# Performance work log

Measured on AMD Instinct MI355X. Metric: run time of the kernel, lower is better.

## Reference

```python
import jax, jax.numpy as jnp
import numpy as np

PATCH_SIZE = [3, 5, 7]
PATCH_SEQ = [5, 7]
SEQ_SIZE = 6
WIN = 210
D_MODEL = 256
B, M = 8, 55
EPS = 1e-5


def _loo(p):
    # leave-one-out index matrix, row i = all indices except i -> (p, p-1)
    return np.array([[k for k in range(p) if k != i] for i in range(p)], dtype=np.int32)


def _mlp(x, W1, b1, W2, b2):
    # torch MLP: fc2(relu(fc1(x))), Linear weights are (out, in)
    h = jax.nn.relu(x @ W1.T + b1)
    return h @ W2.T + b2


def _forward(x, sP, nP, ssP, nsP):
    Bn, L, Mn = x.shape
    # RevIN 'norm' with fresh affine (weight=1, bias=0): identity affine; stats detached
    mean = jax.lax.stop_gradient(jnp.mean(x, axis=1, keepdims=True))
    std = jax.lax.stop_gradient(jnp.sqrt(jnp.var(x, axis=1, keepdims=True) + EPS))
    xn = (x - mean) / std
    xt = jnp.transpose(xn, (0, 2, 1)).reshape(Bn * Mn, L)  # (BM, L)
    sm, pm, ssr, psr = [], [], [], []
    for j, p in enumerate(PATCH_SIZE):
        n = L // p
        x3 = xt.reshape(Bn * Mn, p, n)  # l = r*n + k
        # size branch: leave-one-out over the p axis, blocks ordered i*n + k
        feat = jnp.transpose(x3[:, _loo(p), :], (0, 1, 3, 2)).reshape(Bn * Mn, L, p - 1)
        y = _mlp(feat, *sP[j])[..., 0]  # (BM, L)
        sm.append(jnp.transpose(y.reshape(Bn, Mn, L), (0, 2, 1)))
        # num branch: leave-one-out over the n axis of row l%p, leaving out column l//p
        g = _mlp(x3[:, :, _loo(n)], *nP[j])[..., 0]  # (BM, p, n)
        # torch cats over l (axis 0) then reshapes (B, M, L): flat order is (l, b, m)
        prior = jnp.transpose(g, (2, 1, 0)).reshape(Bn, Mn, L)  # faithful scrambled reshape
        pm.append(jnp.transpose(prior, (0, 2, 1)))
    s = SEQ_SIZE
    for j, p in enumerate(PATCH_SEQ):
        n = L // (p * s)
        x4 = xt.reshape(Bn * Mn, p, n, s)  # l = (r*n + k)*s + t
        # size_seq branch: leave-one-out over p, feature = (p-1)*s per (i, k) position
        feat = jnp.transpose(x4[:, _loo(p)], (0, 1, 3, 2, 4)).reshape(Bn * Mn, p * n, (p - 1) * s)
        y = _mlp(feat, *ssP[j])  # (BM, p*n, s)
        ssr.append(jnp.transpose(y.reshape(Bn, Mn, L), (0, 2, 1)))
        # num_seq branch: leave-one-out over n, cat order i*p + r
        featn = jnp.transpose(x4[:, :, _loo(n), :], (0, 2, 1, 3, 4)).reshape(Bn * Mn, n * p, (n - 1) * s)
        g = _mlp(featn, *nsP[j])  # (BM, n*p, s)
        d0 = PATCH_SEQ[0]  # original code hardcodes patch_seq[0] here
        h = jnp.transpose(g.reshape(Bn, Mn, (n * p) // d0, d0, s), (0, 1, 3, 2, 4)).reshape(Bn, Mn, L)
        psr.append(jnp.transpose(h, (0, 2, 1)))
    # original returns 4 lists of (B, L, M); stack all 10 for a single output
    return jnp.stack(sm + pm + ssr + psr, axis=0)


def setup_inputs() -> dict:
    key = jax.random.key(0)
    keys = iter(jax.random.split(key, 128))
    d = {"x": jax.random.normal(next(keys), (B, WIN, M), dtype=jnp.float32)}

    def lin(name, out_d, in_d):
        d[name + "W"] = jax.random.normal(next(keys), (out_d, in_d), dtype=jnp.float32) / np.float32(np.sqrt(in_d))
        d[name + "b"] = jax.random.normal(next(keys), (out_d,), dtype=jnp.float32) * np.float32(0.01)

    for j, p in enumerate(PATCH_SIZE):
        lin(f"s1_{j}", D_MODEL, p - 1)
        lin(f"s2_{j}", 1, D_MODEL)
        lin(f"n1_{j}", D_MODEL, WIN // p - 1)
        lin(f"n2_{j}", 1, D_MODEL)
    for j, p in enumerate(PATCH_SEQ):
        lin(f"ss1_{j}", D_MODEL, (p - 1) * SEQ_SIZE)
        lin(f"ss2_{j}", SEQ_SIZE, D_MODEL)
        lin(f"ns1_{j}", D_MODEL, WIN // p - SEQ_SIZE)
        lin(f"ns2_{j}", SEQ_SIZE, D_MODEL)
    return d


def reference(x, s1_0W, s1_0b, s2_0W, s2_0b, n1_0W, n1_0b, n2_0W, n2_0b,
              s1_1W, s1_1b, s2_1W, s2_1b, n1_1W, n1_1b, n2_1W, n2_1b,
              s1_2W, s1_2b, s2_2W, s2_2b, n1_2W, n1_2b, n2_2W, n2_2b,
              ss1_0W, ss1_0b, ss2_0W, ss2_0b, ns1_0W, ns1_0b, ns2_0W, ns2_0b,
              ss1_1W, ss1_1b, ss2_1W, ss2_1b, ns1_1W, ns1_1b, ns2_1W, ns2_1b):
    sP = [(s1_0W, s1_0b, s2_0W, s2_0b), (s1_1W, s1_1b, s2_1W, s2_1b), (s1_2W, s1_2b, s2_2W, s2_2b)]
    nP = [(n1_0W, n1_0b, n2_0W, n2_0b), (n1_1W, n1_1b, n2_1W, n2_1b), (n1_2W, n1_2b, n2_2W, n2_2b)]
    ssP = [(ss1_0W, ss1_0b, ss2_0W, ss2_0b), (ss1_1W, ss1_1b, ss2_1W, ss2_1b)]
    nsP = [(ns1_0W, ns1_0b, ns2_0W, ns2_0b), (ns1_1W, ns1_1b, ns2_1W, ns2_1b)]
    return _forward(x, sP, nP, ssP, nsP)
```

## Files before the change

### kernel.cpp

```cpp
#include <hip/hip_runtime.h>

#define LL  210
#define MM  55
#define NBM 440
#define DM  256
#define MLT 11550
#define BLM 92400

#define XTG_OFF  0
#define W1T_OFF  92400
#define REC_OFF  158704

__device__ __forceinline__ void fma4(float4& a, const float4 w, const float s) {
    a.x += w.x * s; a.y += w.y * s; a.z += w.z * s; a.w += w.w * s;
}
__device__ __forceinline__ void fms4(float4& a, const float4 w, const float s) {
    a.x -= w.x * s; a.y -= w.y * s; a.z -= w.z * s; a.w -= w.w * s;
}

__device__ __forceinline__ float bfly8(const float y[8], const int lane) {
    float z[4];
#pragma unroll
    for (int i = 0; i < 4; ++i) {
        float snd = (lane & 1) ? y[2*i] : y[2*i+1];
        float rcv = __shfl_xor(snd, 1, 64);
        z[i] = ((lane & 1) ? y[2*i+1] : y[2*i]) + rcv;
    }
    float u[2];
#pragma unroll
    for (int i = 0; i < 2; ++i) {
        float snd = (lane & 2) ? z[2*i] : z[2*i+1];
        float rcv = __shfl_xor(snd, 2, 64);
        u[i] = ((lane & 2) ? z[2*i+1] : z[2*i]) + rcv;
    }
    {
        float snd = (lane & 4) ? u[0] : u[1];
        float rcv = __shfl_xor(snd, 4, 64);
        float w = ((lane & 4) ? u[1] : u[0]) + rcv;
        w += __shfl_xor(w, 8, 64);
        w += __shfl_xor(w, 16, 64);
        w += __shfl_xor(w, 32, 64);
        return w;
    }
}

__global__ __launch_bounds__(256) void kprep(
        const float* __restrict__ x,
        const float* __restrict__ nw0, const float* __restrict__ nw1, const float* __restrict__ nw2,
        const float* __restrict__ ssw0, const float* __restrict__ ssw1,
        const float* __restrict__ nsw0, const float* __restrict__ nsw1,
        const float* __restrict__ s1W0, const float* __restrict__ s1b0, const float* __restrict__ s2W0,
        const float* __restrict__ s1W1, const float* __restrict__ s1b1, const float* __restrict__ s2W1,
        const float* __restrict__ s1W2, const float* __restrict__ s1b2, const float* __restrict__ s2W2,
        float* __restrict__ xtg, float* __restrict__ w1t, float* __restrict__ recs) {
    const int t = threadIdx.x;
    const int blk = blockIdx.x;
    if (blk < 55) {
        const int mi = t & 7, li = t >> 3;
        const int bm = blk * 8 + mi;
        const int b = bm / MM, m = bm - b * MM;
        const float* xp = x + b * MLT + m;
        float vr[7], s1 = 0.f, s2 = 0.f;
#pragma unroll
        for (int it = 0; it < 7; ++it) {
            const int l = li + 32 * it;
            const float v = (l < LL) ? xp[l * MM] : 0.f;
            vr[it] = v; s1 += v; s2 += v * v;
        }
        s1 += __shfl_xor(s1, 8, 64);  s2 += __shfl_xor(s2, 8, 64);
        s1 += __shfl_xor(s1, 16, 64); s2 += __shfl_xor(s2, 16, 64);
        s1 += __shfl_xor(s1, 32, 64); s2 += __shfl_xor(s2, 32, 64);
        __shared__ float red[2][4][8];
        const int wid = t >> 6, lane = t & 63;
        if (lane < 8) { red[0][wid][lane] = s1; red[1][wid][lane] = s2; }
        __syncthreads();
        const float S1 = red[0][0][mi] + red[0][1][mi] + red[0][2][mi] + red[0][3][mi];
        const float S2 = red[1][0][mi] + red[1][1][mi] + red[1][2][mi] + red[1][3][mi];
        const float mean = S1 * (1.f / 210.f);
        const float inv = rsqrtf(S2 * (1.f / 210.f) - mean * mean + 1e-5f);
        float* xo = xtg + blk * 1680 + mi;
#pragma unroll
        for (int it = 0; it < 7; ++it) {
            const int l = li + 32 * it;
            if (l < LL) xo[l * 8] = (vr[it] - mean) * inv;
        }
    } else if (blk < 55 + 259) {
        const int e = (blk - 55) * 256 + t;
        const int cg = e >> 8, d = e & 255;
        const float* src; int ind, c;
        if (cg < 69)       { src = nw0;  ind = 69; c = cg; }
        else if (cg < 110) { src = nw1;  ind = 41; c = cg - 69; }
        else if (cg < 139) { src = nw2;  ind = 29; c = cg - 110; }
        else if (cg < 163) { src = ssw0; ind = 24; c = cg - 139; }
        else if (cg < 199) { src = ssw1; ind = 36; c = cg - 163; }
        else if (cg < 235) { src = nsw0; ind = 36; c = cg - 199; }
        else               { src = nsw1; ind = 24; c = cg - 235; }
        w1t[cg * DM + d] = src[d * ind + c];
    } else {
        const int e = (blk - 55 - 259) * 256 + t;
        float v;
        if (e < 1024) {
            int d = e >> 2, c = e & 3;
            v = (c < 2) ? s1W0[d * 2 + c] : (c == 2 ? s1b0[d] : s2W0[d]);
        } else if (e < 3072) {
            int rel = e - 1024, d = rel >> 3, c = rel & 7;
            v = (c < 4) ? s1W1[d * 4 + c] : (c == 4 ? s1b1[d] : (c == 5 ? s2W1[d] : 0.f));
        } else {
            int rel = e - 3072, d = rel >> 3, c = rel & 7;
            v = (c < 6) ? s1W2[d * 6 + c] : (c == 6 ? s1b2[d] : s2W2[d]);
        }
        recs[e] = v;
    }
}

template <int IND>
__device__ __forceinline__ void ksize_body2(const float* __restrict__ xtg,
        const float* __restrict__ rec, const float* __restrict__ b2,
        int bm0, int j, float* __restrict__ out) {
    constexpr int N = LL / (IND + 1);
    const int t = threadIdx.x;
    if (t >= LL) return;
    const float* xs = xtg + (bm0 >> 3) * 1680 + (bm0 & 7);
    const int i = t / N, k = t - i * N;
    float2 f[IND];
#pragma unroll
    for (int idx = 0; idx < IND; ++idx) {
        const int row = idx + (idx >= i);
        f[idx] = *(const float2*)&xs[(row * N + k) * 8];
    }
    const float b2v = b2[0];
    float y0a = 0.f, y0b = 0.f, y1a = 0.f, y1b = 0.f;
    const float4* r4 = (const float4*)rec;
    if constexpr (IND == 2) {
#pragma unroll 8
        for (int d = 0; d < DM; d += 2) {
            const float4 a = r4[d], b = r4[d + 1];
            y0a += fmaxf(a.x * f[0].x + a.y * f[1].x + a.z, 0.f) * a.w;
            y1a += fmaxf(a.x * f[0].y + a.y * f[1].y + a.z, 0.f) * a.w;
            y0b += fmaxf(b.x * f[0].x + b.y * f[1].x + b.z, 0.f) * b.w;
            y1b += fmaxf(b.x * f[0].y + b.y * f[1].y + b.z, 0.f) * b.w;
        }
    } else if constexpr (IND == 4) {
#pragma unroll 8
        for (int d = 0; d < DM; d += 2) {
            const float4 a = r4[2*d], b = r4[2*d+1];
            const float4 c = r4[2*d+2], e = r4[2*d+3];
            y0a += fmaxf(a.x*f[0].x + a.y*f[1].x + a.z*f[2].x + a.w*f[3].x + b.x, 0.f) * b.y;
            y1a += fmaxf(a.x*f[0].y + a.y*f[1].y + a.z*f[2].y + a.w*f[3].y + b.x, 0.f) * b.y;
            y0b += fmaxf(c.x*f[0].x + c.y*f[1].x + c.z*f[2].x + c.w*f[3].x + e.x, 0.f) * e.y;
            y1b += fmaxf(c.x*f[0].y + c.y*f[1].y + c.z*f[2].y + c.w*f[3].y + e.x, 0.f) * e.y;
        }
    } else {
#pragma unroll 8
        for (int d = 0; d < DM; d += 2) {
            const float4 a = r4[2*d], b = r4[2*d+1];
            const float4 c = r4[2*d+2], e = r4[2*d+3];
            y0a += fmaxf(a.x*f[0].x + a.y*f[1].x + a.z*f[2].x + a.w*f[3].x + b.x*f[4].x + b.y*f[5].x + b.z, 0.f) * b.w;
            y1a += fmaxf(a.x*f[0].y + a.y*f[1].y + a.z*f[2].y + a.w*f[3].y + b.x*f[4].y + b.y*f[5].y + b.z, 0.f) * b.w;
            y0b += fmaxf(c.x*f[0].x + c.y*f[1].x + c.z*f[2].x + c.w*f[3].x + e.x*f[4].x + e.y*f[5].x + e.z, 0.f) * e.w;
            y1b += fmaxf(c.x*f[0].y + c.y*f[1].y + c.z*f[2].y + c.w*f[3].y + e.x*f[4].y + e.y*f[5].y + e.z, 0.f) * e.w;
        }
    }
#pragma unroll
    for (int g = 0; g < 2; ++g) {
        const int bm = bm0 + g;
        const int b_ = bm / MM, m = bm - b_ * MM;
        const float y = (g ? (y1a + y1b) : (y0a + y0b)) + b2v;
        out[j * BLM + b_ * MLT + t * MM + m] = y;
    }
}

template <int P, int N>
__device__ __forceinline__ void knum_body(const float* __restrict__ xtg,
        const float* __restrict__ wt, const float* __restrict__ b1,
        const float* __restrict__ W2, const float* __restrict__ b2,
        int grp, int r, int j, float* __restrict__ out) {
    const int t = threadIdx.x, wid = t >> 6, lane = t & 63;
    const int g0 = wid * 2;
    const float* xb = xtg + grp * 1680 + r * N * 8 + g0;
    const float4 b1v = *(const float4*)&b1[lane * 4];
    const float4 w2v = *(const float4*)&W2[lane * 4];
    const float b2v = b2[0];
    const float* wl = wt + lane * 4;
    float4 A0 = b1v, A1 = b1v;
    float4 B0 = make_float4(0.f,0.f,0.f,0.f), B1 = B0;
#pragma unroll 4
    for (int q = 1; q < N; ++q) {
        const float4 w = *(const float4*)(wl + (q - 1) * DM);
        const float2 xv = *(const float2*)(xb + q * 8);
        fma4(B0, w, xv.x); fma4(B1, w, xv.y);
    }
    constexpr int NFULL = N / 8, TAIL = N - NFULL * 8;
    for (int c = 0; c <= NFULL; ++c) {
        float y0[8], y1[8];
        const bool full = (c < NFULL);
#pragma unroll
        for (int i = 0; i < 8; ++i) {
            const int k = c * 8 + i;
            if (full || i < TAIL) {
                float hx = fmaxf(A0.x + B0.x, 0.f), hy = fmaxf(A0.y + B0.y, 0.f);
                float hz = fmaxf(A0.z + B0.z, 0.f), hw = fmaxf(A0.w + B0.w, 0.f);
                y0[i] = hx * w2v.x + hy * w2v.y + hz * w2v.z + hw * w2v.w;
                hx = fmaxf(A1.x + B1.x, 0.f); hy = fmaxf(A1.y + B1.y, 0.f);
                hz = fmaxf(A1.z + B1.z, 0.f); hw = fmaxf(A1.w + B1.w, 0.f);
                y1[i] = hx * w2v.x + hy * w2v.y + hz * w2v.z + hw * w2v.w;
                if (full || i < TAIL - 1) {
                    const float4 w = *(const float4*)(wl + k * DM);
                    const float2 xk  = *(const float2*)(xb + k * 8);
                    const float2 xk1 = *(const float2*)(xb + k * 8 + 8);
                    fma4(A0, w, xk.x);  fma4(A1, w, xk.y);
                    fms4(B0, w, xk1.x); fms4(B1, w, xk1.y);
                }
            } else { y0[i] = 0.f; y1[i] = 0.f; }
        }
        const float v0 = bfly8(y0, lane), v1 = bfly8(y1, lane);
        if (lane < 16) {
            const int k = c * 8 + (lane & 7);
            if (k < N) {
                const int bm = grp * 8 + g0 + (lane >> 3);
                const float val = ((lane < 8) ? v0 : v1) + b2v;
                const int fi = (k * P + r) * NBM + bm;
                const int ob = fi / MLT, rem = fi - ob * MLT;
                const int om = rem / LL, ol = rem - om * LL;
                out[(3 + j) * BLM + ob * MLT + ol * MM + om] = val;
            }
        }
    }
}

template <int ISNUM, int P, int N>
__device__ __forceinline__ void kseq_body(const float* __restrict__ xtg,
        const float* __restrict__ w1tb, const float* __restrict__ b1,
        const float* __restrict__ W2, const float* __restrict__ b2,
        int grp, int qc, int slab, float* __restrict__ out) {
    constexpr int NROWS = ISNUM ? (N - 1) : (P - 1);
    const int t = threadIdx.x, wid = t >> 6, lane = t & 63;
    const float4 b1v = *(const float4*)&b1[lane * 4];
    const float* xg = xtg + grp * 1680;
    float b2r[6];
#pragma unroll
    for (int tt = 0; tt < 6; ++tt) b2r[tt] = b2[tt];
    const int bm = grp * 8 + (lane & 7);
    const int b_ = bm / MM, m = bm - b_ * MM;
    const int qe = (qc * 9 + 9 < 35) ? (qc * 9 + 9) : 35;
    for (int q = qc * 9 + wid; q < qe; q += 4) {
        int pivot, fix;
        if (ISNUM) { pivot = q / P; fix = q - pivot * P; }
        else       { pivot = q / N; fix = q - pivot * N; }
        float4 acc[8];
#pragma unroll
        for (int g = 0; g < 8; ++g) acc[g] = b1v;
        const float* wl = w1tb + lane * 4;
        for (int idx = 0; idx < NROWS; ++idx) {
            const int row = idx + (idx >= pivot);
            const int pos0 = ISNUM ? (fix * N + row) * 6 : (row * N + fix) * 6;
            const float* xp = xg + pos0 * 8;
#pragma unroll
            for (int tt = 0; tt < 6; ++tt) {
                const float4 xa = *(const float4*)(xp + tt * 8);
                const float4 xc = *(const float4*)(xp + tt * 8 + 4);
                const float4 w  = *(const float4*)wl; wl += DM;
                fma4(acc[0], w, xa.x); fma4(acc[1], w, xa.y);
                fma4(acc[2], w, xa.z); fma4(acc[3], w, xa.w);
                fma4(acc[4], w, xc.x); fma4(acc[5], w, xc.y);
                fma4(acc[6], w, xc.z); fma4(acc[7], w, xc.w);
            }
        }
#pragma unroll
        for (int g = 0; g < 8; ++g) {
            acc[g].x = fmaxf(acc[g].x, 0.f); acc[g].y = fmaxf(acc[g].y, 0.f);
            acc[g].z = fmaxf(acc[g].z, 0.f); acc[g].w = fmaxf(acc[g].w, 0.f);
        }
        const int c2 = q / 5, dd = q - c2 * 5;
#pragma unroll
        for (int h = 0; h < 2; ++h) {
            float yv0[8], yv1[8], yv2[8];
#pragma unroll
            for (int tt2 = 0; tt2 < 3; ++tt2) {
                const int tt = h * 3 + tt2;
                const float4 w2v = *(const float4*)&W2[tt * DM + lane * 4];
                float* yv = (tt2 == 0) ? yv0 : ((tt2 == 1) ? yv1 : yv2);
#pragma unroll
                for (int g = 0; g < 8; ++g)
                    yv[g] = acc[g].x * w2v.x + acc[g].y * w2v.y + acc[g].z * w2v.z + acc[g].w * w2v.w;
            }
            const float r0 = bfly8(yv0, lane);
            const float r1 = bfly8(yv1, lane);
            const float r2 = bfly8(yv2, lane);
            if (lane < 8) {
#pragma unroll
                for (int tt2 = 0; tt2 < 3; ++tt2) {
                    const int tt = h * 3 + tt2;
                    const int l = ISNUM ? (dd * 42 + c2 * 6 + tt) : (q * 6 + tt);
                    const float rv = (tt2 == 0) ? r0 : ((tt2 == 1) ? r1 : r2);
                    out[slab + b_ * MLT + l * MM + m] = rv + b2r[tt];
                }
            }
        }
    }
}

__global__ __launch_bounds__(256) void kfused(const float* __restrict__ xtg,
        const float* __restrict__ w1t, const float* __restrict__ recs,
        const float* __restrict__ b2s0, const float* __restrict__ b2s1, const float* __restrict__ b2s2,
        const float* __restrict__ nb1_0, const float* __restrict__ nW2_0, const float* __restrict__ nb2_0,
        const float* __restrict__ nb1_1, const float* __restrict__ nW2_1, const float* __restrict__ nb2_1,
        const float* __restrict__ nb1_2, const float* __restrict__ nW2_2, const float* __restrict__ nb2_2,
        const float* __restrict__ ss1b0, const float* __restrict__ ss2W0, const float* __restrict__ ss2b0,
        const float* __restrict__ ss1b1, const float* __restrict__ ss2W1, const float* __restrict__ ss2b1,
        const float* __restrict__ ns1b0, const float* __restrict__ ns2W0, const float* __restrict__ ns2b0,
        const float* __restrict__ ns1b1, const float* __restrict__ ns2W1, const float* __restrict__ ns2b1,
        float* __restrict__ out) {
    const int blk = (int)(((unsigned)blockIdx.x * 997u) % 2365u);
    if (blk < 660) {
        const int j = blk / 220, rel = blk - j * 220;
        const int bm0 = rel * 2;
        if (j == 0)      ksize_body2<2>(xtg, recs,        b2s0, bm0, 0, out);
        else if (j == 1) ksize_body2<4>(xtg, recs + 1024, b2s1, bm0, 1, out);
        else             ksize_body2<6>(xtg, recs + 3072, b2s2, bm0, 2, out);
    } else if (blk < 1485) {
        const int bn = blk - 660;
        if (bn < 165) {
            int rel = bn;       knum_body<3, 70>(xtg, w1t,            nb1_0, nW2_0, nb2_0, rel / 3, rel % 3, 0, out);
        } else if (bn < 440) {
            int rel = bn - 165; knum_body<5, 42>(xtg, w1t + 69 * DM,  nb1_1, nW2_1, nb2_1, rel / 5, rel % 5, 1, out);
        } else {
            int rel = bn - 440; knum_body<7, 30>(xtg, w1t + 110 * DM, nb1_2, nW2_2, nb2_2, rel / 7, rel % 7, 2, out);
        }
    } else {
        const int bs = blk - 1485;
        const int tc = bs / 220, rem = bs - tc * 220;
        const int grp = rem >> 2, qc = rem & 3;
        if (tc == 0)      kseq_body<0, 5, 7>(xtg, w1t + 139 * DM, ss1b0, ss2W0, ss2b0, grp, qc, 6 * BLM, out);
        else if (tc == 1) kseq_body<0, 7, 5>(xtg, w1t + 163 * DM, ss1b1, ss2W1, ss2b1, grp, qc, 7 * BLM, out);
        else if (tc == 2) kseq_body<1, 5, 7>(xtg, w1t + 199 * DM, ns1b0, ns2W0, ns2b0, grp, qc, 8 * BLM, out);
        else              kseq_body<1, 7, 5>(xtg, w1t + 235 * DM, ns1b1, ns2W1, ns2b1, grp, qc, 9 * BLM, out);
    }
}

extern "C" void kernel_launch(void* const* d_in, const int* in_sizes, int n_in,
                              void* d_out, int out_size, void* d_ws, size_t ws_size,
                              hipStream_t stream) {
    (void)in_sizes; (void)n_in; (void)out_size; (void)ws_size;
    const float* x = (const float*)d_in[0];
    const float *s1W[3], *s1b[3], *s2W[3], *s2b[3], *n1W[3], *n1b[3], *n2W[3], *n2b[3];
    for (int j = 0; j < 3; ++j) {
        int base = 1 + j * 8;
        s1W[j] = (const float*)d_in[base + 0]; s1b[j] = (const float*)d_in[base + 1];
        s2W[j] = (const float*)d_in[base + 2]; s2b[j] = (const float*)d_in[base + 3];
        n1W[j] = (const float*)d_in[base + 4]; n1b[j] = (const float*)d_in[base + 5];
        n2W[j] = (const float*)d_in[base + 6]; n2b[j] = (const float*)d_in[base + 7];
    }
    const float *ss1W[2], *ss1b[2], *ss2W[2], *ss2b[2], *ns1W[2], *ns1b[2], *ns2W[2], *ns2b[2];
    for (int j = 0; j < 2; ++j) {
        int base = 25 + j * 8;
        ss1W[j] = (const float*)d_in[base + 0]; ss1b[j] = (const float*)d_in[base + 1];
        ss2W[j] = (const float*)d_in[base + 2]; ss2b[j] = (const float*)d_in[base + 3];
        ns1W[j] = (const float*)d_in[base + 4]; ns1b[j] = (const float*)d_in[base + 5];
        ns2W[j] = (const float*)d_in[base + 6]; ns2b[j] = (const float*)d_in[base + 7];
    }
    float* out  = (float*)d_out;
    float* xtg  = (float*)d_ws + XTG_OFF;
    float* w1t  = (float*)d_ws + W1T_OFF;
    float* recs = (float*)d_ws + REC_OFF;

    kprep<<<334, 256, 0, stream>>>(x,
        n1W[0], n1W[1], n1W[2],
        ss1W[0], ss1W[1], ns1W[0], ns1W[1],
        s1W[0], s1b[0], s2W[0],
        s1W[1], s1b[1], s2W[1],
        s1W[2], s1b[2], s2W[2],
        xtg, w1t, recs);
    kfused<<<2365, 256, 0, stream>>>(xtg, w1t, recs,
        s2b[0], s2b[1], s2b[2],
        n1b[0], n2W[0], n2b[0],
        n1b[1], n2W[1], n2b[1],
        n1b[2], n2W[2], n2b[2],
        ss1b[0], ss2W[0], ss2b[0],
        ss1b[1], ss2W[1], ss2b[1],
        ns1b[0], ns2W[0], ns2b[0],
        ns1b[1], ns2W[1], ns2b[1], out);
}
```

Measured before the change: 229.2 us.

## Process four batch-series per thread in size and num branches, reorder block dispatch

The size-branch and num-branch bodies now handle four (b,m) series per thread instead of two. Each weight vector load from the record table or transposed W1 is reused across four accumulators, and float4 loads replace float2 loads for the inputs. The grid shrinks from 2365 to 1630 blocks. The scrambled blockIdx permutation is replaced by a fixed order: num, then seq, then size. This raises register pressure and leaves fewer blocks to balance load across the device.

Measured after the change: 261.7 us. 1.14x slower.

```diff
diff --git a/kernel.cpp b/kernel.cpp
--- a/kernel.cpp
+++ b/kernel.cpp
@@ -114,7 +114,7 @@
 }
 
 template <int IND>
-__device__ __forceinline__ void ksize_body2(const float* __restrict__ xtg,
+__device__ __forceinline__ void ksize_body4(const float* __restrict__ xtg,
         const float* __restrict__ rec, const float* __restrict__ b2,
         int bm0, int j, float* __restrict__ out) {
     constexpr int N = LL / (IND + 1);
@@ -122,103 +122,126 @@
     if (t >= LL) return;
     const float* xs = xtg + (bm0 >> 3) * 1680 + (bm0 & 7);
     const int i = t / N, k = t - i * N;
-    float2 f[IND];
+    float4 f[IND];
 #pragma unroll
     for (int idx = 0; idx < IND; ++idx) {
         const int row = idx + (idx >= i);
-        f[idx] = *(const float2*)&xs[(row * N + k) * 8];
+        f[idx] = *(const float4*)&xs[(row * N + k) * 8];
     }
     const float b2v = b2[0];
-    float y0a = 0.f, y0b = 0.f, y1a = 0.f, y1b = 0.f;
+    float4 ya = make_float4(0.f,0.f,0.f,0.f), yb = ya;
     const float4* r4 = (const float4*)rec;
     if constexpr (IND == 2) {
-#pragma unroll 8
+#pragma unroll 4
         for (int d = 0; d < DM; d += 2) {
             const float4 a = r4[d], b = r4[d + 1];
-            y0a += fmaxf(a.x * f[0].x + a.y * f[1].x + a.z, 0.f) * a.w;
-            y1a += fmaxf(a.x * f[0].y + a.y * f[1].y + a.z, 0.f) * a.w;
-            y0b += fmaxf(b.x * f[0].x + b.y * f[1].x + b.z, 0.f) * b.w;
-            y1b += fmaxf(b.x * f[0].y + b.y * f[1].y + b.z, 0.f) * b.w;
+            ya.x += fmaxf(a.x*f[0].x + a.y*f[1].x + a.z, 0.f) * a.w;
+            ya.y += fmaxf(a.x*f[0].y + a.y*f[1].y + a.z, 0.f) * a.w;
+            ya.z += fmaxf(a.x*f[0].z + a.y*f[1].z + a.z, 0.f) * a.w;
+            ya.w += fmaxf(a.x*f[0].w + a.y*f[1].w + a.z, 0.f) * a.w;
+            yb.x += fmaxf(b.x*f[0].x + b.y*f[1].x + b.z, 0.f) * b.w;
+            yb.y += fmaxf(b.x*f[0].y + b.y*f[1].y + b.z, 0.f) * b.w;
+            yb.z += fmaxf(b.x*f[0].z + b.y*f[1].z + b.z, 0.f) * b.w;
+            yb.w += fmaxf(b.x*f[0].w + b.y*f[1].w + b.z, 0.f) * b.w;
         }
     } else if constexpr (IND == 4) {
-#pragma unroll 8
+#pragma unroll 4
         for (int d = 0; d < DM; d += 2) {
             const float4 a = r4[2*d], b = r4[2*d+1];
             const float4 c = r4[2*d+2], e = r4[2*d+3];
-            y0a += fmaxf(a.x*f[0].x + a.y*f[1].x + a.z*f[2].x + a.w*f[3].x + b.x, 0.f) * b.y;
-            y1a += fmaxf(a.x*f[0].y + a.y*f[1].y + a.z*f[2].y + a.w*f[3].y + b.x, 0.f) * b.y;
-            y0b += fmaxf(c.x*f[0].x + c.y*f[1].x + c.z*f[2].x + c.w*f[3].x + e.x, 0.f) * e.y;
-            y1b += fmaxf(c.x*f[0].y + c.y*f[1].y + c.z*f[2].y + c.w*f[3].y + e.x, 0.f) * e.y;
+            ya.x += fmaxf(a.x*f[0].x + a.y*f[1].x + a.z*f[2].x + a.w*f[3].x + b.x, 0.f) * b.y;
+            ya.y += fmaxf(a.x*f[0].y + a.y*f[1].y + a.z*f[2].y + a.w*f[3].y + b.x, 0.f) * b.y;
+            ya.z += fmaxf(a.x*f[0].z + a.y*f[1].z + a.z*f[2].z + a.w*f[3].z + b.x, 0.f) * b.y;
+            ya.w += fmaxf(a.x*f[0].w + a.y*f[1].w + a.z*f[2].w + a.w*f[3].w + b.x, 0.f) * b.y;
+            yb.x += fmaxf(c.x*f[0].x + c.y*f[1].x + c.z*f[2].x + c.w*f[3].x + e.x, 0.f) * e.y;
+            yb.y += fmaxf(c.x*f[0].y + c.y*f[1].y + c.z*f[2].y + c.w*f[3].y + e.x, 0.f) * e.y;
+            yb.z += fmaxf(c.x*f[0].z + c.y*f[1].z + c.z*f[2].z + c.w*f[3].z + e.x, 0.f) * e.y;
+            yb.w += fmaxf(c.x*f[0].w + c.y*f[1].w + c.z*f[2].w + c.w*f[3].w + e.x, 0.f) * e.y;
         }
     } else {
-#pragma unroll 8
+#pragma unroll 4
         for (int d = 0; d < DM; d += 2) {
             const float4 a = r4[2*d], b = r4[2*d+1];
             const float4 c = r4[2*d+2], e = r4[2*d+3];
-            y0a += fmaxf(a.x*f[0].x + a.y*f[1].x + a.z*f[2].x + a.w*f[3].x + b.x*f[4].x + b.y*f[5].x + b.z, 0.f) * b.w;
-            y1a += fmaxf(a.x*f[0].y + a.y*f[1].y + a.z*f[2].y + a.w*f[3].y + b.x*f[4].y + b.y*f[5].y + b.z, 0.f) * b.w;
-            y0b += fmaxf(c.x*f[0].x + c.y*f[1].x + c.z*f[2].x + c.w*f[3].x + e.x*f[4].x + e.y*f[5].x + e.z, 0.f) * e.w;
-            y1b += fmaxf(c.x*f[0].y + c.y*f[1].y + c.z*f[2].y + c.w*f[3].y + e.x*f[4].y + e.y*f[5].y + e.z, 0.f) * e.w;
-        }
-    }
-#pragma unroll
-    for (int g = 0; g < 2; ++g) {
+            ya.x += fmaxf(a.x*f[0].x + a.y*f[1].x + a.z*f[2].x + a.w*f[3].x + b.x*f[4].x + b.y*f[5].x + b.z, 0.f) * b.w;
+            ya.y += fmaxf(a.x*f[0].y + a.y*f[1].y + a.z*f[2].y + a.w*f[3].y + b.x*f[4].y + b.y*f[5].y + b.z, 0.f) * b.w;
+            ya.z += fmaxf(a.x*f[0].z + a.y*f[1].z + a.z*f[2].z + a.w*f[3].z + b.x*f[4].z + b.y*f[5].z + b.z, 0.f) * b.w;
+            ya.w += fmaxf(a.x*f[0].w + a.y*f[1].w + a.z*f[2].w + a.w*f[3].w + b.x*f[4].w + b.y*f[5].w + b.z, 0.f) * b.w;
+            yb.x += fmaxf(c.x*f[0].x + c.y*f[1].x + c.z*f[2].x + c.w*f[3].x + e.x*f[4].x + e.y*f[5].x + e.z, 0.f) * e.w;
+            yb.y += fmaxf(c.x*f[0].y + c.y*f[1].y + c.z*f[2].y + c.w*f[3].y + e.x*f[4].y + e.y*f[5].y + e.z, 0.f) * e.w;
+            yb.z += fmaxf(c.x*f[0].z + c.y*f[1].z + c.z*f[2].z + c.w*f[3].z + e.x*f[4].z + e.y*f[5].z + e.z, 0.f) * e.w;
+            yb.w += fmaxf(c.x*f[0].w + c.y*f[1].w + c.z*f[2].w + c.w*f[3].w + e.x*f[4].w + e.y*f[5].w + e.z, 0.f) * e.w;
+        }
+    }
+    const float yv[4] = { ya.x + yb.x, ya.y + yb.y, ya.z + yb.z, ya.w + yb.w };
+#pragma unroll
+    for (int g = 0; g < 4; ++g) {
         const int bm = bm0 + g;
         const int b_ = bm / MM, m = bm - b_ * MM;
-        const float y = (g ? (y1a + y1b) : (y0a + y0b)) + b2v;
-        out[j * BLM + b_ * MLT + t * MM + m] = y;
+        out[j * BLM + b_ * MLT + t * MM + m] = yv[g] + b2v;
     }
 }
 
 template <int P, int N>
-__device__ __forceinline__ void knum_body(const float* __restrict__ xtg,
+__device__ __forceinline__ void knum_body4(const float* __restrict__ xtg,
         const float* __restrict__ wt, const float* __restrict__ b1,
         const float* __restrict__ W2, const float* __restrict__ b2,
-        int grp, int r, int j, float* __restrict__ out) {
+        int grp0, int r, int j, float* __restrict__ out) {
     const int t = threadIdx.x, wid = t >> 6, lane = t & 63;
-    const int g0 = wid * 2;
+    const int grp = grp0 + (wid >> 1);
+    if (grp >= 55) return;
+    const int g0 = (wid & 1) * 4;
     const float* xb = xtg + grp * 1680 + r * N * 8 + g0;
     const float4 b1v = *(const float4*)&b1[lane * 4];
     const float4 w2v = *(const float4*)&W2[lane * 4];
     const float b2v = b2[0];
     const float* wl = wt + lane * 4;
-    float4 A0 = b1v, A1 = b1v;
-    float4 B0 = make_float4(0.f,0.f,0.f,0.f), B1 = B0;
-#pragma unroll 4
+    float4 A0 = b1v, A1 = b1v, A2 = b1v, A3 = b1v;
+    float4 B0 = make_float4(0.f,0.f,0.f,0.f), B1 = B0, B2 = B0, B3 = B0;
+#pragma unroll 2
     for (int q = 1; q < N; ++q) {
         const float4 w = *(const float4*)(wl + (q - 1) * DM);
-        const float2 xv = *(const float2*)(xb + q * 8);
-        fma4(B0, w, xv.x); fma4(B1, w, xv.y);
+        const float4 xv = *(const float4*)(xb + q * 8);
+        fma4(B0, w, xv.x); fma4(B1, w, xv.y); fma4(B2, w, xv.z); fma4(B3, w, xv.w);
     }
     constexpr int NFULL = N / 8, TAIL = N - NFULL * 8;
     for (int c = 0; c <= NFULL; ++c) {
-        float y0[8], y1[8];
+        float y0[8], y1[8], y2[8], y3[8];
         const bool full = (c < NFULL);
 #pragma unroll
         for (int i = 0; i < 8; ++i) {
             const int k = c * 8 + i;
             if (full || i < TAIL) {
-                float hx = fmaxf(A0.x + B0.x, 0.f), hy = fmaxf(A0.y + B0.y, 0.f);
-                float hz = fmaxf(A0.z + B0.z, 0.f), hw = fmaxf(A0.w + B0.w, 0.f);
+                float hx, hy, hz, hw;
+                hx = fmaxf(A0.x + B0.x, 0.f); hy = fmaxf(A0.y + B0.y, 0.f);
+                hz = fmaxf(A0.z + B0.z, 0.f); hw = fmaxf(A0.w + B0.w, 0.f);
                 y0[i] = hx * w2v.x + hy * w2v.y + hz * w2v.z + hw * w2v.w;
                 hx = fmaxf(A1.x + B1.x, 0.f); hy = fmaxf(A1.y + B1.y, 0.f);
                 hz = fmaxf(A1.z + B1.z, 0.f); hw = fmaxf(A1.w + B1.w, 0.f);
                 y1[i] = hx * w2v.x + hy * w2v.y + hz * w2v.z + hw * w2v.w;
+                hx = fmaxf(A2.x + B2.x, 0.f); hy = fmaxf(A2.y + B2.y, 0.f);
+                hz = fmaxf(A2.z + B2.z, 0.f); hw = fmaxf(A2.w + B2.w, 0.f);
+                y2[i] = hx * w2v.x + hy * w2v.y + hz * w2v.z + hw * w2v.w;
+                hx = fmaxf(A3.x + B3.x, 0.f); hy = fmaxf(A3.y + B3.y, 0.f);
+                hz = fmaxf(A3.z + B3.z, 0.f); hw = fmaxf(A3.w + B3.w, 0.f);
+                y3[i] = hx * w2v.x + hy * w2v.y + hz * w2v.z + hw * w2v.w;
                 if (full || i < TAIL - 1) {
-                    const float4 w = *(const float4*)(wl + k * DM);
-                    const float2 xk  = *(const float2*)(xb + k * 8);
-                    const float2 xk1 = *(const float2*)(xb + k * 8 + 8);
-                    fma4(A0, w, xk.x);  fma4(A1, w, xk.y);
-                    fms4(B0, w, xk1.x); fms4(B1, w, xk1.y);
+                    const float4 w   = *(const float4*)(wl + k * DM);
+                    const float4 xk  = *(const float4*)(xb + k * 8);
+                    const float4 xk1 = *(const float4*)(xb + k * 8 + 8);
+                    fma4(A0, w, xk.x);  fma4(A1, w, xk.y);  fma4(A2, w, xk.z);  fma4(A3, w, xk.w);
+                    fms4(B0, w, xk1.x); fms4(B1, w, xk1.y); fms4(B2, w, xk1.z); fms4(B3, w, xk1.w);
                 }
-            } else { y0[i] = 0.f; y1[i] = 0.f; }
+            } else { y0[i] = 0.f; y1[i] = 0.f; y2[i] = 0.f; y3[i] = 0.f; }
         }
         const float v0 = bfly8(y0, lane), v1 = bfly8(y1, lane);
-        if (lane < 16) {
+        const float v2 = bfly8(y2, lane), v3 = bfly8(y3, lane);
+        if (lane < 32) {
             const int k = c * 8 + (lane & 7);
             if (k < N) {
-                const int bm = grp * 8 + g0 + (lane >> 3);
-                const float val = ((lane < 8) ? v0 : v1) + b2v;
+                const int s = lane >> 3;
+                const int bm = grp * 8 + g0 + s;
+                const float val = ((s == 0) ? v0 : (s == 1) ? v1 : (s == 2) ? v2 : v3) + b2v;
                 const int fi = (k * P + r) * NBM + bm;
                 const int ob = fi / MLT, rem = fi - ob * MLT;
                 const int om = rem / LL, ol = rem - om * LL;
@@ -311,30 +334,35 @@
         const float* __restrict__ ns1b0, const float* __restrict__ ns2W0, const float* __restrict__ ns2b0,
         const float* __restrict__ ns1b1, const float* __restrict__ ns2W1, const float* __restrict__ ns2b1,
         float* __restrict__ out) {
-    const int blk = (int)(((unsigned)blockIdx.x * 997u) % 2365u);
-    if (blk < 660) {
-        const int j = blk / 220, rel = blk - j * 220;
-        const int bm0 = rel * 2;
-        if (j == 0)      ksize_body2<2>(xtg, recs,        b2s0, bm0, 0, out);
-        else if (j == 1) ksize_body2<4>(xtg, recs + 1024, b2s1, bm0, 1, out);
-        else             ksize_body2<6>(xtg, recs + 3072, b2s2, bm0, 2, out);
-    } else if (blk < 1485) {
-        const int bn = blk - 660;
-        if (bn < 165) {
-            int rel = bn;       knum_body<3, 70>(xtg, w1t,            nb1_0, nW2_0, nb2_0, rel / 3, rel % 3, 0, out);
-        } else if (bn < 440) {
-            int rel = bn - 165; knum_body<5, 42>(xtg, w1t + 69 * DM,  nb1_1, nW2_1, nb2_1, rel / 5, rel % 5, 1, out);
+    const int blk = blockIdx.x;
+    if (blk < 420) {
+        if (blk < 84) {
+            const int r = blk % 3, grp0 = (blk / 3) * 2;
+            knum_body4<3, 70>(xtg, w1t,            nb1_0, nW2_0, nb2_0, grp0, r, 0, out);
+        } else if (blk < 224) {
+            const int bn = blk - 84;
+            const int r = bn % 5, grp0 = (bn / 5) * 2;
+            knum_body4<5, 42>(xtg, w1t + 69 * DM,  nb1_1, nW2_1, nb2_1, grp0, r, 1, out);
         } else {
-            int rel = bn - 440; knum_body<7, 30>(xtg, w1t + 110 * DM, nb1_2, nW2_2, nb2_2, rel / 7, rel % 7, 2, out);
-        }
-    } else {
-        const int bs = blk - 1485;
+            const int bn = blk - 224;
+            const int r = bn % 7, grp0 = (bn / 7) * 2;
+            knum_body4<7, 30>(xtg, w1t + 110 * DM, nb1_2, nW2_2, nb2_2, grp0, r, 2, out);
+        }
+    } else if (blk < 1300) {
+        const int bs = blk - 420;
         const int tc = bs / 220, rem = bs - tc * 220;
         const int grp = rem >> 2, qc = rem & 3;
         if (tc == 0)      kseq_body<0, 5, 7>(xtg, w1t + 139 * DM, ss1b0, ss2W0, ss2b0, grp, qc, 6 * BLM, out);
         else if (tc == 1) kseq_body<0, 7, 5>(xtg, w1t + 163 * DM, ss1b1, ss2W1, ss2b1, grp, qc, 7 * BLM, out);
         else if (tc == 2) kseq_body<1, 5, 7>(xtg, w1t + 199 * DM, ns1b0, ns2W0, ns2b0, grp, qc, 8 * BLM, out);
         else              kseq_body<1, 7, 5>(xtg, w1t + 235 * DM, ns1b1, ns2W1, ns2b1, grp, qc, 9 * BLM, out);
+    } else {
+        const int bs = blk - 1300;
+        const int j = bs / 110, rel = bs - j * 110;
+        const int bm0 = rel * 4;
+        if (j == 0)      ksize_body4<2>(xtg, recs,        b2s0, bm0, 0, out);
+        else if (j == 1) ksize_body4<4>(xtg, recs + 1024, b2s1, bm0, 1, out);
+        else             ksize_body4<6>(xtg, recs + 3072, b2s2, bm0, 2, out);
     }
 }
 
@@ -371,7 +399,7 @@
         s1W[1], s1b[1], s2W[1],
         s1W[2], s1b[2], s2W[2],
         xtg, w1t, recs);
-    kfused<<<2365, 256, 0, stream>>>(xtg, w1t, recs,
+    kfused<<<1630, 256, 0, stream>>>(xtg, w1t, recs,
         s2b[0], s2b[1], s2b[2],
         n1b[0], n2W[0], n2b[0],
         n1b[1], n2W[1], n2b[1],
```

## Split fused kernel work into finer blocks for more parallelism

Applied to the files above, without the earlier changes.

The size branch now processes one bm per block instead of two. The num branch splits each (group, r) task into two halves over the k range, with the second half precomputing its starting accumulator. The seq branch uses 7 q-chunks of 5 instead of 4 of 9, and the blockIdx scramble is removed. The grid grows from 2365 to 4510 blocks to improve load balance and latency hiding, at the cost of duplicated weight loads, extra prologue work, and lost per-thread reuse of weights across two bm values.

New measurement: 226.3 us. About the same (-1.3%).

```diff
diff --git a/kernel.cpp b/kernel.cpp
--- a/kernel.cpp
+++ b/kernel.cpp
@@ -114,67 +114,58 @@
 }
 
 template <int IND>
-__device__ __forceinline__ void ksize_body2(const float* __restrict__ xtg,
+__device__ __forceinline__ void ksize_body(const float* __restrict__ xtg,
         const float* __restrict__ rec, const float* __restrict__ b2,
-        int bm0, int j, float* __restrict__ out) {
+        int bm, int j, float* __restrict__ out) {
     constexpr int N = LL / (IND + 1);
     const int t = threadIdx.x;
     if (t >= LL) return;
-    const float* xs = xtg + (bm0 >> 3) * 1680 + (bm0 & 7);
+    const float* xs = xtg + (bm >> 3) * 1680 + (bm & 7);
     const int i = t / N, k = t - i * N;
-    float2 f[IND];
+    float f[IND];
 #pragma unroll
     for (int idx = 0; idx < IND; ++idx) {
-        const int row = idx + (idx >= i);
-        f[idx] = *(const float2*)&xs[(row * N + k) * 8];
-    }
-    const float b2v = b2[0];
-    float y0a = 0.f, y0b = 0.f, y1a = 0.f, y1b = 0.f;
+        int row = idx + (idx >= i);
+        f[idx] = xs[(row * N + k) * 8];
+    }
+    float y0 = b2[0], y1 = 0.f;
     const float4* r4 = (const float4*)rec;
     if constexpr (IND == 2) {
 #pragma unroll 8
         for (int d = 0; d < DM; d += 2) {
             const float4 a = r4[d], b = r4[d + 1];
-            y0a += fmaxf(a.x * f[0].x + a.y * f[1].x + a.z, 0.f) * a.w;
-            y1a += fmaxf(a.x * f[0].y + a.y * f[1].y + a.z, 0.f) * a.w;
-            y0b += fmaxf(b.x * f[0].x + b.y * f[1].x + b.z, 0.f) * b.w;
-            y1b += fmaxf(b.x * f[0].y + b.y * f[1].y + b.z, 0.f) * b.w;
+            y0 += fmaxf(a.x * f[0] + a.y * f[1] + a.z, 0.f) * a.w;
+            y1 += fmaxf(b.x * f[0] + b.y * f[1] + b.z, 0.f) * b.w;
         }
     } else if constexpr (IND == 4) {
 #pragma unroll 8
         for (int d = 0; d < DM; d += 2) {
             const float4 a = r4[2*d], b = r4[2*d+1];
             const float4 c = r4[2*d+2], e = r4[2*d+3];
-            y0a += fmaxf(a.x*f[0].x + a.y*f[1].x + a.z*f[2].x + a.w*f[3].x + b.x, 0.f) * b.y;
-            y1a += fmaxf(a.x*f[0].y + a.y*f[1].y + a.z*f[2].y + a.w*f[3].y + b.x, 0.f) * b.y;
-            y0b += fmaxf(c.x*f[0].x + c.y*f[1].x + c.z*f[2].x + c.w*f[3].x + e.x, 0.f) * e.y;
-            y1b += fmaxf(c.x*f[0].y + c.y*f[1].y + c.z*f[2].y + c.w*f[3].y + e.x, 0.f) * e.y;
+            y0 += fmaxf(a.x*f[0] + a.y*f[1] + a.z*f[2] + a.w*f[3] + b.x, 0.f) * b.y;
+            y1 += fmaxf(c.x*f[0] + c.y*f[1] + c.z*f[2] + c.w*f[3] + e.x, 0.f) * e.y;
         }
     } else {
 #pragma unroll 8
         for (int d = 0; d < DM; d += 2) {
             const float4 a = r4[2*d], b = r4[2*d+1];
             const float4 c = r4[2*d+2], e = r4[2*d+3];
-            y0a += fmaxf(a.x*f[0].x + a.y*f[1].x + a.z*f[2].x + a.w*f[3].x + b.x*f[4].x + b.y*f[5].x + b.z, 0.f) * b.w;
-            y1a += fmaxf(a.x*f[0].y + a.y*f[1].y + a.z*f[2].y + a.w*f[3].y + b.x*f[4].y + b.y*f[5].y + b.z, 0.f) * b.w;
-            y0b += fmaxf(c.x*f[0].x + c.y*f[1].x + c.z*f[2].x + c.w*f[3].x + e.x*f[4].x + e.y*f[5].x + e.z, 0.f) * e.w;
-            y1b += fmaxf(c.x*f[0].y + c.y*f[1].y + c.z*f[2].y + c.w*f[3].y + e.x*f[4].y + e.y*f[5].y + e.z, 0.f) * e.w;
-        }
-    }
-#pragma unroll
-    for (int g = 0; g < 2; ++g) {
-        const int bm = bm0 + g;
-        const int b_ = bm / MM, m = bm - b_ * MM;
-        const float y = (g ? (y1a + y1b) : (y0a + y0b)) + b2v;
-        out[j * BLM + b_ * MLT + t * MM + m] = y;
-    }
-}
-
-template <int P, int N>
-__device__ __forceinline__ void knum_body(const float* __restrict__ xtg,
+            y0 += fmaxf(a.x*f[0] + a.y*f[1] + a.z*f[2] + a.w*f[3] + b.x*f[4] + b.y*f[5] + b.z, 0.f) * b.w;
+            y1 += fmaxf(c.x*f[0] + c.y*f[1] + c.z*f[2] + c.w*f[3] + e.x*f[4] + e.y*f[5] + e.z, 0.f) * e.w;
+        }
+    }
+    const int b_ = bm / MM, m = bm - b_ * MM;
+    out[j * BLM + b_ * MLT + t * MM + m] = y0 + y1;
+}
+
+template <int P, int N, int HALF>
+__device__ __forceinline__ void knum_bodyH(const float* __restrict__ xtg,
         const float* __restrict__ wt, const float* __restrict__ b1,
         const float* __restrict__ W2, const float* __restrict__ b2,
         int grp, int r, int j, float* __restrict__ out) {
+    constexpr int KS  = HALF ? (N / 2) : 0;
+    constexpr int KE  = HALF ? N : (N / 2);
+    constexpr int CNT = KE - KS;
     const int t = threadIdx.x, wid = t >> 6, lane = t & 63;
     const int g0 = wid * 2;
     const float* xb = xtg + grp * 1680 + r * N * 8 + g0;
@@ -185,18 +176,24 @@
     float4 A0 = b1v, A1 = b1v;
     float4 B0 = make_float4(0.f,0.f,0.f,0.f), B1 = B0;
 #pragma unroll 4
-    for (int q = 1; q < N; ++q) {
+    for (int q = 0; q < KS; ++q) {
+        const float4 w = *(const float4*)(wl + q * DM);
+        const float2 xv = *(const float2*)(xb + q * 8);
+        fma4(A0, w, xv.x); fma4(A1, w, xv.y);
+    }
+#pragma unroll 4
+    for (int q = KS + 1; q < N; ++q) {
         const float4 w = *(const float4*)(wl + (q - 1) * DM);
         const float2 xv = *(const float2*)(xb + q * 8);
         fma4(B0, w, xv.x); fma4(B1, w, xv.y);
     }
-    constexpr int NFULL = N / 8, TAIL = N - NFULL * 8;
+    constexpr int NFULL = CNT / 8, TAIL = CNT - NFULL * 8;
     for (int c = 0; c <= NFULL; ++c) {
         float y0[8], y1[8];
         const bool full = (c < NFULL);
 #pragma unroll
         for (int i = 0; i < 8; ++i) {
-            const int k = c * 8 + i;
+            const int k = KS + c * 8 + i;
             if (full || i < TAIL) {
                 float hx = fmaxf(A0.x + B0.x, 0.f), hy = fmaxf(A0.y + B0.y, 0.f);
                 float hz = fmaxf(A0.z + B0.z, 0.f), hw = fmaxf(A0.w + B0.w, 0.f);
@@ -215,8 +212,9 @@
         }
         const float v0 = bfly8(y0, lane), v1 = bfly8(y1, lane);
         if (lane < 16) {
-            const int k = c * 8 + (lane & 7);
-            if (k < N) {
+            const int krel = c * 8 + (lane & 7);
+            if (krel < CNT) {
+                const int k = KS + krel;
                 const int bm = grp * 8 + g0 + (lane >> 3);
                 const float val = ((lane < 8) ? v0 : v1) + b2v;
                 const int fi = (k * P + r) * NBM + bm;
@@ -242,8 +240,8 @@
     for (int tt = 0; tt < 6; ++tt) b2r[tt] = b2[tt];
     const int bm = grp * 8 + (lane & 7);
     const int b_ = bm / MM, m = bm - b_ * MM;
-    const int qe = (qc * 9 + 9 < 35) ? (qc * 9 + 9) : 35;
-    for (int q = qc * 9 + wid; q < qe; q += 4) {
+    const int qs = qc * 5;
+    for (int q = qs + wid; q < qs + 5; q += 4) {
         int pivot, fix;
         if (ISNUM) { pivot = q / P; fix = q - pivot * P; }
         else       { pivot = q / N; fix = q - pivot * N; }
@@ -311,26 +309,35 @@
         const float* __restrict__ ns1b0, const float* __restrict__ ns2W0, const float* __restrict__ ns2b0,
         const float* __restrict__ ns1b1, const float* __restrict__ ns2W1, const float* __restrict__ ns2b1,
         float* __restrict__ out) {
-    const int blk = (int)(((unsigned)blockIdx.x * 997u) % 2365u);
-    if (blk < 660) {
-        const int j = blk / 220, rel = blk - j * 220;
-        const int bm0 = rel * 2;
-        if (j == 0)      ksize_body2<2>(xtg, recs,        b2s0, bm0, 0, out);
-        else if (j == 1) ksize_body2<4>(xtg, recs + 1024, b2s1, bm0, 1, out);
-        else             ksize_body2<6>(xtg, recs + 3072, b2s2, bm0, 2, out);
-    } else if (blk < 1485) {
-        const int bn = blk - 660;
-        if (bn < 165) {
-            int rel = bn;       knum_body<3, 70>(xtg, w1t,            nb1_0, nW2_0, nb2_0, rel / 3, rel % 3, 0, out);
-        } else if (bn < 440) {
-            int rel = bn - 165; knum_body<5, 42>(xtg, w1t + 69 * DM,  nb1_1, nW2_1, nb2_1, rel / 5, rel % 5, 1, out);
+    const int blk = blockIdx.x;
+    if (blk < 1320) {
+        if (blk < NBM)          ksize_body<2>(xtg, recs,        b2s0, blk,           0, out);
+        else if (blk < 2 * NBM) ksize_body<4>(xtg, recs + 1024, b2s1, blk - NBM,     1, out);
+        else                    ksize_body<6>(xtg, recs + 3072, b2s2, blk - 2 * NBM, 2, out);
+    } else if (blk < 2970) {
+        const int bn = blk - 1320;
+        if (bn < 330) {
+            const int pair = bn >> 1, half = bn & 1;
+            const int grp = pair / 3, r = pair - grp * 3;
+            if (half == 0) knum_bodyH<3, 70, 0>(xtg, w1t, nb1_0, nW2_0, nb2_0, grp, r, 0, out);
+            else           knum_bodyH<3, 70, 1>(xtg, w1t, nb1_0, nW2_0, nb2_0, grp, r, 0, out);
+        } else if (bn < 880) {
+            const int x = bn - 330;
+            const int pair = x >> 1, half = x & 1;
+            const int grp = pair / 5, r = pair - grp * 5;
+            if (half == 0) knum_bodyH<5, 42, 0>(xtg, w1t + 69 * DM, nb1_1, nW2_1, nb2_1, grp, r, 1, out);
+            else           knum_bodyH<5, 42, 1>(xtg, w1t + 69 * DM, nb1_1, nW2_1, nb2_1, grp, r, 1, out);
         } else {
-            int rel = bn - 440; knum_body<7, 30>(xtg, w1t + 110 * DM, nb1_2, nW2_2, nb2_2, rel / 7, rel % 7, 2, out);
+            const int x = bn - 880;
+            const int pair = x >> 1, half = x & 1;
+            const int grp = pair / 7, r = pair - grp * 7;
+            if (half == 0) knum_bodyH<7, 30, 0>(xtg, w1t + 110 * DM, nb1_2, nW2_2, nb2_2, grp, r, 2, out);
+            else           knum_bodyH<7, 30, 1>(xtg, w1t + 110 * DM, nb1_2, nW2_2, nb2_2, grp, r, 2, out);
         }
     } else {
-        const int bs = blk - 1485;
-        const int tc = bs / 220, rem = bs - tc * 220;
-        const int grp = rem >> 2, qc = rem & 3;
+        const int bs = blk - 2970;
+        const int tc = bs / 385, rem = bs - tc * 385;
+        const int grp = rem / 7, qc = rem - grp * 7;
         if (tc == 0)      kseq_body<0, 5, 7>(xtg, w1t + 139 * DM, ss1b0, ss2W0, ss2b0, grp, qc, 6 * BLM, out);
         else if (tc == 1) kseq_body<0, 7, 5>(xtg, w1t + 163 * DM, ss1b1, ss2W1, ss2b1, grp, qc, 7 * BLM, out);
         else if (tc == 2) kseq_body<1, 5, 7>(xtg, w1t + 199 * DM, ns1b0, ns2W0, ns2b0, grp, qc, 8 * BLM, out);
@@ -371,7 +378,7 @@
         s1W[1], s1b[1], s2W[1],
         s1W[2], s1b[2], s2W[2],
         xtg, w1t, recs);
-    kfused<<<2365, 256, 0, stream>>>(xtg, w1t, recs,
+    kfused<<<4510, 256, 0, stream>>>(xtg, w1t, recs,
         s2b[0], s2b[1], s2b[2],
         n1b[0], n2W[0], n2b[0],
         n1b[1], n2W[1], n2b[1],
```
